# Kernel tuning notes

Measured on AMD Instinct MI355X. Metric: run time of the kernel, lower is better.

Reference implementation:

```python
import jax, jax.numpy as jnp
import numpy as np

HEADS = 16
HEAD_SIZE = 64
INF = 1e12  # bert4keras K.infinity() uses a large finite value


def _rotate_interleaved(x):
    # result[..., 2i] = -x[..., 2i+1]; result[..., 2i+1] = x[..., 2i]
    x2 = jnp.stack([-x[..., 1::2], x[..., ::2]], axis=-1)
    return x2.reshape(x.shape)


def setup_inputs() -> dict:
    key = jax.random.key(0)
    k1, k2 = jax.random.split(key)
    B, N, D = 8, 1024, 1024
    x = jax.random.normal(k1, (B, N, D), dtype=jnp.float32)
    W = jax.random.normal(k2, (D, 2 * HEADS * HEAD_SIZE), dtype=jnp.float32) * (1.0 / np.sqrt(D))
    b = jnp.zeros((2 * HEADS * HEAD_SIZE,), dtype=jnp.float32)
    seq_mask = jnp.ones((B, N), dtype=jnp.float32)
    return {"x": x, "W": W, "b": b, "seq_mask": seq_mask}


def reference(x, W, b, seq_mask):
    B, N, _ = x.shape
    H, d = HEADS, HEAD_SIZE
    proj = x @ W + b                       # [B, N, 2*H*d]
    z = proj.reshape(B, N, H, 2 * d)       # split into heads then stack
    qw, kw = z[..., :d], z[..., d:]        # [B, N, H, d]

    # RoPE (interleaved sin/cos)
    pos = jnp.arange(N, dtype=jnp.float32)
    freqs = jnp.power(10000.0, -2.0 * jnp.arange(d // 2, dtype=jnp.float32) / d)
    ang = pos[:, None] * freqs[None, :]    # [N, d/2]
    cos_pos = jnp.repeat(jnp.cos(ang), 2, axis=-1)[None, :, None, :]  # [1,N,1,d]
    sin_pos = jnp.repeat(jnp.sin(ang), 2, axis=-1)[None, :, None, :]
    qw = qw * cos_pos + _rotate_interleaved(qw) * sin_pos
    kw = kw * cos_pos + _rotate_interleaved(kw) * sin_pos

    logits = jnp.einsum('bmhd,bnhd->bhmn', qw, kw)   # [B, H, N, N]

    # sequence masking on query (axis 2) and key (axis 3)
    logits = logits - (1.0 - seq_mask[:, None, :, None]) * INF
    logits = logits - (1.0 - seq_mask[:, None, None, :]) * INF

    # triangular mask: keep upper triangle including diagonal
    tri = jnp.triu(jnp.ones((N, N), dtype=logits.dtype))
    logits = logits - (1.0 - tri) * INF
    return logits / jnp.sqrt(jnp.float32(d))
```

## Files before the change

kernel.cpp:

```cpp
#include <hip/hip_runtime.h>

typedef __bf16 bf16;
typedef __bf16 bf16x4 __attribute__((ext_vector_type(4)));
typedef __bf16 bf16x8 __attribute__((ext_vector_type(8)));
typedef float f32x4 __attribute__((ext_vector_type(4)));

#define GL(p) ((const __attribute__((address_space(1))) void*)(p))
#define LD(p) ((__attribute__((address_space(3))) void*)(p))

static __device__ __forceinline__ void nt_store4(float* p, f32x4 v) {
    __builtin_nontemporal_store(v, (f32x4*)p);
}

__global__ __launch_bounds__(256) void k_prep(
    const float4* __restrict__ x4, bf16x4* __restrict__ o4,
    const float* __restrict__ W, bf16* __restrict__ Wt,
    float* __restrict__ cost, float* __restrict__ sint)
{
    __shared__ bf16 tile[64][65];
    const int bid = (int)blockIdx.x;
    const int t = threadIdx.x;
    if (bid < 2048) {
        for (int i = bid * 256 + t; i < 2097152; i += 2048 * 256) {
            float4 v = x4[i];
            bf16x4 o;
            o[0] = (bf16)v.x; o[1] = (bf16)v.y; o[2] = (bf16)v.z; o[3] = (bf16)v.w;
            o4[i] = o;
        }
    } else if (bid < 2560) {
        const int wid = bid - 2048;
        const int k0 = (wid & 15) * 64;
        const int n0 = (wid >> 4) * 64;
        const int c = t & 63, r4 = t >> 6;
#pragma unroll
        for (int p = 0; p < 16; ++p) {
            int r = p * 4 + r4;
            tile[r][c] = (bf16)W[(size_t)(k0 + r) * 2048 + n0 + c];
        }
        __syncthreads();
#pragma unroll
        for (int p = 0; p < 16; ++p) {
            int n = p * 4 + r4;
            Wt[(size_t)(n0 + n) * 1024 + k0 + c] = tile[c][n];
        }
    } else {
        int idx = (bid - 2560) * 256 + t;
        int pos = idx >> 5, i = idx & 31;
        float freq = powf(10000.f, -(float)i / 32.f);
        float ang = (float)pos * freq;
        cost[idx] = cosf(ang);
        sint[idx] = sinf(ang);
    }
}

__global__ __launch_bounds__(512) void k_gemm1(
    const bf16* __restrict__ Xb, const bf16* __restrict__ Wt,
    const float* __restrict__ bias,
    const float* __restrict__ cost, const float* __restrict__ sint,
    bf16* __restrict__ Qb, bf16* __restrict__ Kb)
{
    __shared__ bf16 lA[2][256 * 64];
    __shared__ bf16 lB[2][128 * 64];
    const int t = threadIdx.x;
    const int lane = t & 63;
    const int wave = t >> 6;
    const int wr = (wave >> 1) * 64;
    const int wc = (wave & 1) * 64;
    const int bm = (int)blockIdx.x * 256;
    const int bn = (int)blockIdx.y * 128;
    const int rl = lane & 15;
    const int hi = lane >> 4;

    f32x4 acc[4][4] = {};

#define STAGE1(kt, c) do {                                                              \
    _Pragma("unroll")                                                                   \
    for (int p = 0; p < 4; ++p) {                                                       \
        int e = t * 8 + p * 4096;                                                       \
        int row = e >> 6; int g = (e >> 3) & 7;                                         \
        __builtin_amdgcn_global_load_lds(                                               \
            GL(Xb + (size_t)(bm + row) * 1024 + (kt) * 64 + ((g ^ (row & 7)) << 3)),    \
            LD(&lA[c][e]), 16, 0, 0);                                                   \
    }                                                                                   \
    _Pragma("unroll")                                                                   \
    for (int p = 0; p < 2; ++p) {                                                       \
        int e = t * 8 + p * 4096;                                                       \
        int row = e >> 6; int g = (e >> 3) & 7;                                         \
        __builtin_amdgcn_global_load_lds(                                               \
            GL(Wt + (size_t)(bn + row) * 1024 + (kt) * 64 + ((g ^ (row & 7)) << 3)),    \
            LD(&lB[c][e]), 16, 0, 0);                                                   \
    }                                                                                   \
} while (0)

    STAGE1(0, 0);
    STAGE1(1, 1);
    asm volatile("s_waitcnt vmcnt(6)" ::: "memory");
    __builtin_amdgcn_sched_barrier(0);
    __builtin_amdgcn_s_barrier();
    asm volatile("" ::: "memory");

    for (int kt = 0; kt < 16; ++kt) {
        const int cur = kt & 1;
        bf16x8 af[2][4], bfr[2][4];
#pragma unroll
        for (int ks = 0; ks < 2; ++ks) {
#pragma unroll
            for (int m = 0; m < 4; ++m) {
                int R = wr + m * 16 + rl;
                af[ks][m] = *(const bf16x8*)&lA[cur][(R << 6) + (((ks * 4 + hi) ^ (R & 7)) << 3)];
            }
#pragma unroll
            for (int n = 0; n < 4; ++n) {
                int S = wc + n * 16 + rl;
                bfr[ks][n] = *(const bf16x8*)&lB[cur][(S << 6) + (((ks * 4 + hi) ^ (S & 7)) << 3)];
            }
        }
#pragma unroll
        for (int ks = 0; ks < 2; ++ks)
#pragma unroll
            for (int m = 0; m < 4; ++m)
#pragma unroll
                for (int n = 0; n < 4; ++n)
                    acc[m][n] = __builtin_amdgcn_mfma_f32_16x16x32_bf16(af[ks][m], bfr[ks][n], acc[m][n], 0, 0, 0);

        if (kt < 15) {
            __builtin_amdgcn_s_barrier();
            if (kt + 2 < 16) {
                STAGE1(kt + 2, cur);
                asm volatile("s_waitcnt vmcnt(6)" ::: "memory");
            } else {
                asm volatile("s_waitcnt vmcnt(0)" ::: "memory");
            }
            __builtin_amdgcn_sched_barrier(0);
            __builtin_amdgcn_s_barrier();
            asm volatile("" ::: "memory");
        }
    }
#undef STAGE1

#pragma unroll
    for (int m = 0; m < 4; ++m) {
#pragma unroll
        for (int n = 0; n < 4; ++n) {
            int colg = bn + wc + n * 16 + rl;
            float bv = bias[colg];
            int h = colg >> 7;
            int rem = colg & 127;
            int qk = rem >> 6;
            int dcol = rem & 63;
            int fi = dcol >> 1;
            float sgn = (dcol & 1) ? 1.f : -1.f;
            bf16* dstb = qk ? Kb : Qb;
#pragma unroll
            for (int r = 0; r < 4; ++r) {
                int rowg = bm + wr + m * 16 + hi * 4 + r;
                int pos = rowg & 1023, bidx = rowg >> 10;
                float val = acc[m][n][r] + bv;
                float part = __shfl_xor(val, 1);
                float cv = cost[pos * 32 + fi], sv = sint[pos * 32 + fi];
                float outv = val * cv + sgn * part * sv;
                dstb[(((size_t)(bidx * 16 + h)) * 1024 + pos) * 64 + dcol] = (bf16)outv;
            }
        }
    }
}

__global__ __launch_bounds__(256) void k_gemm2(
    const bf16* __restrict__ Qb, const bf16* __restrict__ Kb,
    const float* __restrict__ smask, float* __restrict__ out)
{
    __shared__ __align__(16) char smem[33792];
    bf16* lQ = (bf16*)smem;
    bf16* lK = (bf16*)(smem + 16384);
    float* ldsF = (float*)smem;
    float* npen_l = (float*)(smem + 32768);
    float* mpen_l = (float*)(smem + 33280);

    const int t = threadIdx.x;
    const int lane = t & 63, wave = t >> 6;
    const int wm = (wave >> 1) * 64, wn = (wave & 1) * 64;
    const int bid = (int)blockIdx.x;
    const int xcd = bid & 7;
    const int idx0 = bid >> 3;
    const int bh = xcd * 16 + (idx0 & 15);
    const int tile = idx0 >> 4;
    const int bm = (tile >> 3) * 128;
    const int bn = (tile & 7) * 128;
    const int b = bh >> 4;
    const int rl = lane & 15, hi = lane >> 4;
    const float NINF = 1.25e11f;

    if (t < 128) npen_l[t] = 1.f - smask[b * 1024 + bn + t];
    else         mpen_l[t - 128] = 1.f - smask[b * 1024 + bm + (t - 128)];

    if (bn + 128 <= bm) {
        __syncthreads();
#pragma unroll
        for (int it = 0; it < 16; ++it) {
            int idx = it * 256 + t;
            int lr = idx >> 5;
            int col = (idx & 31) << 2;
            float mp = mpen_l[lr];
            f32x4 np = *(const f32x4*)&npen_l[col];
            f32x4 v;
#pragma unroll
            for (int r = 0; r < 4; ++r) v[r] = -(mp + np[r] + 1.f) * NINF;
            nt_store4(&out[((size_t)bh << 20) + ((size_t)(bm + lr) << 10) + bn + col], v);
        }
        return;
    }

    const size_t qoff = (size_t)bh * 1024 * 64;
#pragma unroll
    for (int p = 0; p < 4; ++p) {
        int e = t * 8 + p * 2048;
        int gr = e >> 3;
        int row = gr >> 3, c16 = gr & 7;
        int se = (row << 6) + ((c16 ^ (row & 7)) << 3);
        __builtin_amdgcn_global_load_lds(GL(Qb + qoff + (size_t)bm * 64 + se), LD(&lQ[e]), 16, 0, 0);
        __builtin_amdgcn_global_load_lds(GL(Kb + qoff + (size_t)bn * 64 + se), LD(&lK[e]), 16, 0, 0);
    }
    __syncthreads();

    f32x4 acc[4][4] = {};
#pragma unroll
    for (int ks = 0; ks < 2; ++ks) {
        bf16x8 af[4], bq[4];
#pragma unroll
        for (int i = 0; i < 4; ++i) {
            int R = wn + i * 16 + rl;
            af[i] = *(const bf16x8*)&lK[(R << 6) + ((((ks << 2) + hi) ^ (R & 7)) << 3)];
        }
#pragma unroll
        for (int j = 0; j < 4; ++j) {
            int Rq = wm + j * 16 + rl;
            bq[j] = *(const bf16x8*)&lQ[(Rq << 6) + ((((ks << 2) + hi) ^ (Rq & 7)) << 3)];
        }
#pragma unroll
        for (int i = 0; i < 4; ++i)
#pragma unroll
            for (int j = 0; j < 4; ++j)
                acc[i][j] = __builtin_amdgcn_mfma_f32_16x16x32_bf16(af[i], bq[j], acc[i][j], 0, 0, 0);
    }
    __syncthreads();

    for (int P = 0; P < 2; ++P) {
        if ((wave >> 1) == P) {
#pragma unroll
            for (int i = 0; i < 4; ++i)
#pragma unroll
                for (int j = 0; j < 4; ++j) {
                    int lrow = j * 16 + rl;
                    int lcol4 = wn * 4 + i * 64 + hi * 16;
                    char* p = (char*)ldsF + (lrow << 9) + (lcol4 ^ ((lrow & 7) << 4));
                    *(f32x4*)p = acc[i][j];
                }
        }
        __syncthreads();
#pragma unroll
        for (int k = 0; k < 8; ++k) {
            int idx = k * 256 + t;
            int lr = idx >> 5, slot = idx & 31;
            f32x4 v = ((const f32x4*)ldsF)[idx];
            int col = (((slot << 4) ^ ((lr & 7) << 4)) >> 2);
            int grow = bm + P * 64 + lr;
            int gcol = bn + col;
            float mp = mpen_l[P * 64 + lr];
            f32x4 np = *(const f32x4*)&npen_l[col];
            f32x4 vo;
#pragma unroll
            for (int r = 0; r < 4; ++r) {
                float pen = mp + np[r] + ((gcol + r < grow) ? 1.f : 0.f);
                vo[r] = v[r] * 0.125f - pen * NINF;
            }
            nt_store4(&out[((size_t)bh << 20) + ((size_t)grow << 10) + gcol], vo);
        }
        __syncthreads();
    }
}

extern "C" void kernel_launch(void* const* d_in, const int* in_sizes, int n_in,
                              void* d_out, int out_size, void* d_ws, size_t ws_size,
                              hipStream_t stream) {
    (void)in_sizes; (void)n_in; (void)out_size; (void)ws_size;
    const float* x    = (const float*)d_in[0];
    const float* W    = (const float*)d_in[1];
    const float* bias = (const float*)d_in[2];
    const float* sm   = (const float*)d_in[3];
    float* out = (float*)d_out;

    char* ws = (char*)d_ws;
    size_t o = 0;
    bf16* Xb = (bf16*)(ws + o); o += 8388608ull * 2;
    bf16* Wt = (bf16*)(ws + o); o += 2097152ull * 2;
    bf16* Qb = (bf16*)(ws + o); o += 8388608ull * 2;
    bf16* Kb = (bf16*)(ws + o); o += 8388608ull * 2;
    float* cost = (float*)(ws + o); o += 32768ull * 4;
    float* sint = (float*)(ws + o); o += 32768ull * 4;

    hipLaunchKernelGGL(k_prep, dim3(2688), dim3(256), 0, stream,
                       (const float4*)x, (bf16x4*)Xb, W, Wt, cost, sint);
    hipLaunchKernelGGL(k_gemm1, dim3(32, 16), dim3(512), 0, stream,
                       Xb, Wt, bias, cost, sint, Qb, Kb);
    hipLaunchKernelGGL(k_gemm2, dim3(8192), dim3(256), 0, stream,
                       Qb, Kb, sm, out);
}
```

Measured before the change: 164.8 us.

## Move lower-triangle mask fill into projection GEMM to overlap with compute

The fully masked lower-triangle output tiles, which are pure constant stores, are now written by the first GEMM kernel, interleaved with its k-loop iterations. The second kernel only launches blocks for upper-triangle and diagonal tiles, using a triangular index mapping. The goal is to overlap the large store-bound mask writes with the compute-bound projection GEMM and to remove the wasted blocks from the second launch. The cost is extra store traffic inside the GEMM main loop, which may disturb its LDS and VMEM scheduling.

```diff
diff --git a/kernel.cpp b/kernel.cpp
--- a/kernel.cpp
+++ b/kernel.cpp
@@ -57,7 +57,8 @@
     const bf16* __restrict__ Xb, const bf16* __restrict__ Wt,
     const float* __restrict__ bias,
     const float* __restrict__ cost, const float* __restrict__ sint,
-    bf16* __restrict__ Qb, bf16* __restrict__ Kb)
+    bf16* __restrict__ Qb, bf16* __restrict__ Kb,
+    const float* __restrict__ smask, float* __restrict__ out)
 {
     __shared__ bf16 lA[2][256 * 64];
     __shared__ bf16 lB[2][128 * 64];
@@ -70,6 +71,8 @@
     const int bn = (int)blockIdx.y * 128;
     const int rl = lane & 15;
     const int hi = lane >> 4;
+    const int flat7 = ((int)blockIdx.y * 32 + (int)blockIdx.x) * 7;
+    const float NINF = 1.25e11f;
 
     f32x4 acc[4][4] = {};
 
@@ -101,6 +104,29 @@
 
     for (int kt = 0; kt < 16; ++kt) {
         const int cur = kt & 1;
+
+        if (kt < 14) {
+            int inst = flat7 + (kt >> 1);
+            int bh2 = inst & 127;
+            int k28 = inst >> 7;
+            int tm = 1;
+            while (k28 >= ((tm * (tm + 1)) >> 1)) ++tm;
+            int tn = k28 - ((tm * (tm - 1)) >> 1);
+            int b2 = bh2 >> 4;
+            int s0 = (kt & 1) * 4;
+#pragma unroll
+            for (int s = 0; s < 4; ++s) {
+                int pos = (s0 + s) * 512 + t;
+                int row = pos >> 5, c4 = (pos & 31) << 2;
+                float smm = smask[b2 * 1024 + tm * 128 + row];
+                f32x4 smn = *(const f32x4*)&smask[b2 * 1024 + tn * 128 + c4];
+                f32x4 v;
+#pragma unroll
+                for (int r = 0; r < 4; ++r) v[r] = (smm + smn[r] - 3.f) * NINF;
+                nt_store4(&out[((size_t)bh2 << 20) + ((size_t)(tm * 128 + row) << 10) + tn * 128 + c4], v);
+            }
+        }
+
         bf16x8 af[2][4], bfr[2][4];
 #pragma unroll
         for (int ks = 0; ks < 2; ++ks) {
@@ -183,32 +209,18 @@
     const int xcd = bid & 7;
     const int idx0 = bid >> 3;
     const int bh = xcd * 16 + (idx0 & 15);
-    const int tile = idx0 >> 4;
-    const int bm = (tile >> 3) * 128;
-    const int bn = (tile & 7) * 128;
+    int rem36 = idx0 >> 4;
+    int tm = 0;
+    while (rem36 >= 8 - tm) { rem36 -= 8 - tm; ++tm; }
+    const int tn = tm + rem36;
+    const int bm = tm * 128;
+    const int bn = tn * 128;
     const int b = bh >> 4;
     const int rl = lane & 15, hi = lane >> 4;
     const float NINF = 1.25e11f;
 
     if (t < 128) npen_l[t] = 1.f - smask[b * 1024 + bn + t];
     else         mpen_l[t - 128] = 1.f - smask[b * 1024 + bm + (t - 128)];
-
-    if (bn + 128 <= bm) {
-        __syncthreads();
-#pragma unroll
-        for (int it = 0; it < 16; ++it) {
-            int idx = it * 256 + t;
-            int lr = idx >> 5;
-            int col = (idx & 31) << 2;
-            float mp = mpen_l[lr];
-            f32x4 np = *(const f32x4*)&npen_l[col];
-            f32x4 v;
-#pragma unroll
-            for (int r = 0; r < 4; ++r) v[r] = -(mp + np[r] + 1.f) * NINF;
-            nt_store4(&out[((size_t)bh << 20) + ((size_t)(bm + lr) << 10) + bn + col], v);
-        }
-        return;
-    }
 
     const size_t qoff = (size_t)bh * 1024 * 64;
 #pragma unroll
@@ -301,7 +313,7 @@
     hipLaunchKernelGGL(k_prep, dim3(2688), dim3(256), 0, stream,
                        (const float4*)x, (bf16x4*)Xb, W, Wt, cost, sint);
     hipLaunchKernelGGL(k_gemm1, dim3(32, 16), dim3(512), 0, stream,
-                       Xb, Wt, bias, cost, sint, Qb, Kb);
-    hipLaunchKernelGGL(k_gemm2, dim3(8192), dim3(256), 0, stream,
+                       Xb, Wt, bias, cost, sint, Qb, Kb, sm, out);
+    hipLaunchKernelGGL(k_gemm2, dim3(4608), dim3(256), 0, stream,
                        Qb, Kb, sm, out);
 }
```

After: 166.4 us. About the same (+0.9%).
